# Kernel tuning notes

Hardware: AMD Instinct MI355X
Metric: run time of the kernel (lower is better)

The kernel has to match this reference:

```python
import jax, jax.numpy as jnp
import numpy as np

D = 512          # d_model
S = D // 2       # d_state
NL = 6           # num_layers
EVERY = 4        # attention_every
WIN = 256        # window_size
H = 8            # num_heads
DH = D // H      # head_dim
EPS = 1e-5


def layer_norm(x, gamma, beta):
    mu = jnp.mean(x, axis=-1, keepdims=True)
    var = jnp.mean((x - mu) ** 2, axis=-1, keepdims=True)
    return (x - mu) * jax.lax.rsqrt(var + EPS) * gamma + beta


def mamba_layer(seq, state, conv_w, Wx, Wh, Wout, A):
    """Lightweight Mamba-style update returning a (B, D) state summary.

    causal depthwise conv (k=3) -> SiLU -> project to d_state -> diagonal
    linear SSM scan (computed in closed form since the decay is constant)
    -> read out final state back to d_model.
    """
    B, L, _ = seq.shape
    xp = jnp.pad(seq, ((0, 0), (2, 0), (0, 0)))  # causal pad, kernel 3
    x = conv_w[0] * xp[:, :L] + conv_w[1] * xp[:, 1:L + 1] + conv_w[2] * xp[:, 2:L + 2]
    x = jax.nn.silu(x)
    u = jnp.einsum('bld,ds->bls', x, Wx)          # (B, L, S)
    a = jax.nn.sigmoid(A)                          # (S,) decay in (0,1)
    powers = (L - 1) - jnp.arange(L, dtype=jnp.float32)  # (L,)
    w = a[None, :] ** powers[:, None]              # (L, S)
    h0 = state @ Wh                                # (B, S)
    hT = (a ** L) * h0 + jnp.einsum('bls,ls->bs', u, w)
    return hT @ Wout                               # (B, D)


def local_attention(seq, Wqkv, bqkv, Wo, bo):
    B, L, _ = seq.shape
    qkv = seq @ Wqkv.T + bqkv                      # (B, L, 3D)
    q, k, v = jnp.split(qkv, 3, axis=-1)
    q = q.reshape(B, L, H, DH).transpose(0, 2, 1, 3)
    k = k.reshape(B, L, H, DH).transpose(0, 2, 1, 3)
    v = v.reshape(B, L, H, DH).transpose(0, 2, 1, 3)
    idx = jnp.arange(L)
    band = jnp.abs(idx[:, None] - idx[None, :]) <= WIN
    mask = jnp.where(band, 0.0, -jnp.inf).astype(seq.dtype)  # (L, L)
    scores = jnp.einsum('bhqd,bhkd->bhqk', q, k) / np.sqrt(DH) + mask
    attn = jax.nn.softmax(scores, axis=-1)
    out = jnp.einsum('bhqk,bhkd->bhqd', attn, v)
    out = out.transpose(0, 2, 1, 3).reshape(B, L, D)
    return out @ Wo.T + bo


def setup_inputs() -> dict:
    key = jax.random.key(0)
    ks = jax.random.split(key, 12)
    B, L = 4, 2048
    sc = 0.02
    return {
        'context': jax.random.normal(ks[0], (B, L, D), jnp.float32),
        'conv_w': jax.random.normal(ks[1], (NL, 3, D), jnp.float32) * sc,
        'Wx': jax.random.normal(ks[2], (NL, D, S), jnp.float32) * sc,
        'Wh': jax.random.normal(ks[3], (NL, D, S), jnp.float32) * sc,
        'Wout': jax.random.normal(ks[4], (NL, S, D), jnp.float32) * sc,
        'A': jax.random.normal(ks[5], (NL, S), jnp.float32),
        'gamma_m': jnp.ones((D,), jnp.float32),
        'beta_m': jnp.zeros((D,), jnp.float32),
        'gamma_a': jnp.ones((D,), jnp.float32),
        'beta_a': jnp.zeros((D,), jnp.float32),
        'Wqkv': jax.random.normal(ks[6], (3 * D, D), jnp.float32) * sc,
        'bqkv': jnp.zeros((3 * D,), jnp.float32),
        'Wo': jax.random.normal(ks[7], (D, D), jnp.float32) * sc,
        'bo': jnp.zeros((D,), jnp.float32),
    }


def reference(context, conv_w, Wx, Wh, Wout, A, gamma_m, beta_m, gamma_a, beta_a, Wqkv, bqkv, Wo, bo):
    B = context.shape[0]
    seq = context
    state = jnp.zeros((B, D), context.dtype)  # initial_state=None
    for i in range(NL):
        state = mamba_layer(seq, state, conv_w[i], Wx[i], Wh[i], Wout[i], A[i])
        seq = layer_norm(seq + state[:, None, :], gamma_m, beta_m)
        if (i + 1) % EVERY == 0:
            attn_out = local_attention(seq, Wqkv, bqkv, Wo, bo)
            seq = layer_norm(seq + attn_out, gamma_a, beta_a)
    return seq
```

## Files before the change

### kernel.cpp

```cpp
#include <hip/hip_runtime.h>

#define B_ 4
#define L_ 2048
#define D_ 512
#define S_ 256
#define H_ 8
#define DH_ 64
#define WIN_ 256
#define EPS_ 1e-5f
#define LOG2E_ 1.4426950408889634f
#define UWIN_ 768
#define UCHUNKS_ 6

using f32x4 = __attribute__((ext_vector_type(4))) float;
using s16x8 = __attribute__((ext_vector_type(8))) short;

__device__ __forceinline__ unsigned short f2b(float f) {
  unsigned int u = __builtin_bit_cast(unsigned int, f);
  u += 0x7FFFu + ((u >> 16) & 1u);
  return (unsigned short)(u >> 16);
}

__device__ __forceinline__ float silu(float y) { return y / (1.f + expf(-y)); }

__device__ __forceinline__ void gll16(const void* g, void* l) {
  __builtin_amdgcn_global_load_lds((const __attribute__((address_space(1))) void*)g,
                                   (__attribute__((address_space(3))) void*)l, 16, 0, 0);
}

__global__ __launch_bounds__(256) void k_f2b(const float* __restrict__ in,
                                             unsigned short* __restrict__ out, int n4) {
  int i = blockIdx.x * 256 + threadIdx.x;
  if (i >= n4) return;
  float4 v = reinterpret_cast<const float4*>(in)[i];
  ushort4 o;
  o.x = f2b(v.x); o.y = f2b(v.y); o.z = f2b(v.z); o.w = f2b(v.w);
  reinterpret_cast<ushort4*>(out)[i] = o;
}

__global__ void k_twx(const float* __restrict__ wx, unsigned short* __restrict__ wxt) {
  __shared__ float tile[32][33];
  int lyr = blockIdx.z;
  int d0 = blockIdx.x * 32, s0 = blockIdx.y * 32;
  const float* src = wx + (size_t)lyr * D_ * S_;
  unsigned short* dst = wxt + (size_t)lyr * S_ * D_;
  for (int r = threadIdx.y; r < 32; r += 8)
    tile[r][threadIdx.x] = src[(size_t)(d0 + r) * S_ + s0 + threadIdx.x];
  __syncthreads();
  for (int r = threadIdx.y; r < 32; r += 8)
    dst[(size_t)(s0 + r) * D_ + d0 + threadIdx.x] = f2b(tile[threadIdx.x][r]);
}

__global__ __launch_bounds__(128) void k_conv_silu(const float* __restrict__ seq,
                                                   const float* __restrict__ cw,
                                                   unsigned short* __restrict__ x) {
  int bl = blockIdx.x;
  int l = bl & (L_ - 1);
  int t = threadIdx.x;
  const float4* s4 = reinterpret_cast<const float4*>(seq);
  const float4* c4 = reinterpret_cast<const float4*>(cw);
  size_t row = (size_t)bl * 128;
  float4 c0 = c4[t], c1 = c4[128 + t], c2 = c4[256 + t];
  float4 z = make_float4(0.f, 0.f, 0.f, 0.f);
  float4 s0 = (l >= 2) ? s4[row - 256 + t] : z;
  float4 s1 = (l >= 1) ? s4[row - 128 + t] : z;
  float4 s2 = s4[row + t];
  float y0 = c0.x * s0.x + c1.x * s1.x + c2.x * s2.x;
  float y1 = c0.y * s0.y + c1.y * s1.y + c2.y * s2.y;
  float y2 = c0.z * s0.z + c1.z * s1.z + c2.z * s2.z;
  float y3 = c0.w * s0.w + c1.w * s1.w + c2.w * s2.w;
  ushort4 o;
  o.x = f2b(silu(y0)); o.y = f2b(silu(y1)); o.z = f2b(silu(y2)); o.w = f2b(silu(y3));
  reinterpret_cast<ushort4*>(x)[row + t] = o;
}

__global__ __launch_bounds__(64) void k_lnconv(const float* __restrict__ seqIn,
                                               const float* __restrict__ add, int addfull,
                                               const float* __restrict__ gamma,
                                               const float* __restrict__ beta,
                                               float* __restrict__ seqOut,
                                               unsigned short* __restrict__ xbf,
                                               const float* __restrict__ cw,
                                               unsigned short* __restrict__ sbf) {
  int t = threadIdx.x;
  int r0 = blockIdx.x * 8;
  int b = r0 >> 11, l0 = r0 & (L_ - 1);
  bool hasconv = (cw != nullptr);
  const float4* in4 = reinterpret_cast<const float4*>(seqIn);
  const float4* ad4 = reinterpret_cast<const float4*>(add);
  float4* out4 = reinterpret_cast<float4*>(seqOut);
  float4 g0 = reinterpret_cast<const float4*>(gamma)[2 * t];
  float4 g1 = reinterpret_cast<const float4*>(gamma)[2 * t + 1];
  float4 be0 = reinterpret_cast<const float4*>(beta)[2 * t];
  float4 be1 = reinterpret_cast<const float4*>(beta)[2 * t + 1];
  float4 av0, av1;
  if (!addfull) { av0 = ad4[b * 128 + 2 * t]; av1 = ad4[b * 128 + 2 * t + 1]; }
  float4 c0a, c0b, c1a, c1b, c2a, c2b;
  if (hasconv) {
    const float4* c4 = reinterpret_cast<const float4*>(cw);
    c0a = c4[2 * t]; c0b = c4[2 * t + 1];
    c1a = c4[128 + 2 * t]; c1b = c4[128 + 2 * t + 1];
    c2a = c4[256 + 2 * t]; c2b = c4[256 + 2 * t + 1];
  }
  float4 z = make_float4(0.f, 0.f, 0.f, 0.f);
  float4 m2a = z, m2b = z, m1a = z, m1b = z;
  int nrows = hasconv ? 10 : 8;
  int lstart = hasconv ? l0 - 2 : l0;
  for (int j = 0; j < nrows; ++j) {
    int l = lstart + j;
    float4 oa = z, ob = z;
    if (l >= 0) {
      size_t r4 = ((size_t)(b * L_ + l)) * 128;
      float4 v0 = in4[r4 + 2 * t], v1 = in4[r4 + 2 * t + 1];
      float4 a0, a1;
      if (addfull) { a0 = ad4[r4 + 2 * t]; a1 = ad4[r4 + 2 * t + 1]; }
      else { a0 = av0; a1 = av1; }
      v0.x += a0.x; v0.y += a0.y; v0.z += a0.z; v0.w += a0.w;
      v1.x += a1.x; v1.y += a1.y; v1.z += a1.z; v1.w += a1.w;
      float sx = v0.x + v0.y + v0.z + v0.w + v1.x + v1.y + v1.z + v1.w;
      float sq = v0.x * v0.x + v0.y * v0.y + v0.z * v0.z + v0.w * v0.w +
                 v1.x * v1.x + v1.y * v1.y + v1.z * v1.z + v1.w * v1.w;
#pragma unroll
      for (int off = 1; off < 64; off <<= 1) {
        sx += __shfl_xor(sx, off);
        sq += __shfl_xor(sq, off);
      }
      float mu = sx * (1.f / D_);
      float var = sq * (1.f / D_) - mu * mu;
      float rstd = rsqrtf(var + EPS_);
      oa.x = (v0.x - mu) * rstd * g0.x + be0.x;
      oa.y = (v0.y - mu) * rstd * g0.y + be0.y;
      oa.z = (v0.z - mu) * rstd * g0.z + be0.z;
      oa.w = (v0.w - mu) * rstd * g0.w + be0.w;
      ob.x = (v1.x - mu) * rstd * g1.x + be1.x;
      ob.y = (v1.y - mu) * rstd * g1.y + be1.y;
      ob.z = (v1.z - mu) * rstd * g1.z + be1.z;
      ob.w = (v1.w - mu) * rstd * g1.w + be1.w;
      if (l >= l0) {
        out4[r4 + 2 * t] = oa;
        out4[r4 + 2 * t + 1] = ob;
        if (sbf) {
          s16x8 sb;
          sb[0] = (short)f2b(oa.x); sb[1] = (short)f2b(oa.y);
          sb[2] = (short)f2b(oa.z); sb[3] = (short)f2b(oa.w);
          sb[4] = (short)f2b(ob.x); sb[5] = (short)f2b(ob.y);
          sb[6] = (short)f2b(ob.z); sb[7] = (short)f2b(ob.w);
          *reinterpret_cast<s16x8*>(sbf + ((size_t)(b * L_ + l)) * 512 + t * 8) = sb;
        }
      }
    }
    if (hasconv && j >= 2) {
      float y0 = c0a.x * m2a.x + c1a.x * m1a.x + c2a.x * oa.x;
      float y1 = c0a.y * m2a.y + c1a.y * m1a.y + c2a.y * oa.y;
      float y2 = c0a.z * m2a.z + c1a.z * m1a.z + c2a.z * oa.z;
      float y3 = c0a.w * m2a.w + c1a.w * m1a.w + c2a.w * oa.w;
      float y4 = c0b.x * m2b.x + c1b.x * m1b.x + c2b.x * ob.x;
      float y5 = c0b.y * m2b.y + c1b.y * m1b.y + c2b.y * ob.y;
      float y6 = c0b.z * m2b.z + c1b.z * m1b.z + c2b.z * ob.z;
      float y7 = c0b.w * m2b.w + c1b.w * m1b.w + c2b.w * ob.w;
      s16x8 xo;
      xo[0] = (short)f2b(silu(y0)); xo[1] = (short)f2b(silu(y1));
      xo[2] = (short)f2b(silu(y2)); xo[3] = (short)f2b(silu(y3));
      xo[4] = (short)f2b(silu(y4)); xo[5] = (short)f2b(silu(y5));
      xo[6] = (short)f2b(silu(y6)); xo[7] = (short)f2b(silu(y7));
      *reinterpret_cast<s16x8*>(xbf + ((size_t)(b * L_ + l)) * 512 + t * 8) = xo;
    }
    m2a = m1a; m2b = m1b; m1a = oa; m1b = ob;
  }
}

__device__ __forceinline__ void g128_core(const unsigned short* __restrict__ A,
                                          const unsigned short* __restrict__ Bt,
                                          int K, int m0, int n0, int k_lo, int k_hi,
                                          unsigned short* As, unsigned short* Bs,
                                          f32x4 (&acc)[4][4]) {
  int t = threadIdx.x;
  int lane = t & 63;
  int g = lane >> 4, mr = lane & 15;
  int wid = t >> 6, wr = wid >> 1, wc = wid & 1;
#pragma unroll
  for (int i = 0; i < 4; ++i)
#pragma unroll
    for (int j = 0; j < 4; ++j) { f32x4 z = {0.f, 0.f, 0.f, 0.f}; acc[i][j] = z; }
  int r0 = t >> 2, c4 = t & 3;
  int p = ((c4 ^ (r0 & 3)) << 3);
  const unsigned short* ag0 = A + (size_t)(m0 + r0) * K + p;
  const unsigned short* ag1 = ag0 + (size_t)64 * K;
  const unsigned short* bg0 = Bt + (size_t)(n0 + r0) * K + p;
  const unsigned short* bg1 = bg0 + (size_t)64 * K;
  int woff = wid * 512;
  int sa = ((g ^ (mr & 3)) << 3);
  gll16(ag0 + k_lo, As + woff);
  gll16(ag1 + k_lo, As + 2048 + woff);
  gll16(bg0 + k_lo, Bs + woff);
  gll16(bg1 + k_lo, Bs + 2048 + woff);
  int nsteps = (k_hi - k_lo) >> 5;
  int cur = 0;
  for (int s = 0; s < nsteps; ++s) {
    int k0 = k_lo + (s << 5);
    if (s + 1 < nsteps) {
      int nb = (cur ^ 1) * 4096;
      gll16(ag0 + k0 + 32, As + nb + woff);
      gll16(ag1 + k0 + 32, As + nb + 2048 + woff);
      gll16(bg0 + k0 + 32, Bs + nb + woff);
      gll16(bg1 + k0 + 32, Bs + nb + 2048 + woff);
      asm volatile("s_waitcnt vmcnt(4)" ::: "memory");
    } else {
      asm volatile("s_waitcnt vmcnt(0)" ::: "memory");
    }
    __builtin_amdgcn_sched_barrier(0);
    __builtin_amdgcn_s_barrier();
    __builtin_amdgcn_sched_barrier(0);
    const unsigned short* Ar = As + cur * 4096;
    const unsigned short* Br = Bs + cur * 4096;
    s16x8 af[4], bf[4];
#pragma unroll
    for (int fm = 0; fm < 4; ++fm)
      af[fm] = *reinterpret_cast<const s16x8*>(Ar + (size_t)(wr * 64 + fm * 16 + mr) * 32 + sa);
#pragma unroll
    for (int fn = 0; fn < 4; ++fn)
      bf[fn] = *reinterpret_cast<const s16x8*>(Br + (size_t)(wc * 64 + fn * 16 + mr) * 32 + sa);
#pragma unroll
    for (int fm = 0; fm < 4; ++fm)
#pragma unroll
      for (int fn = 0; fn < 4; ++fn)
        acc[fm][fn] = __builtin_amdgcn_mfma_f32_16x16x32_bf16(af[fm], bf[fn], acc[fm][fn], 0, 0, 0);
    __builtin_amdgcn_sched_barrier(0);
    __builtin_amdgcn_s_barrier();
    cur ^= 1;
  }
}

__global__ __launch_bounds__(256) void k_g128(const unsigned short* __restrict__ A,
                                              const unsigned short* __restrict__ Bt,
                                              float* __restrict__ C,
                                              const float* __restrict__ bias,
                                              int N, int K) {
  __shared__ __align__(16) unsigned short As[8192], Bs[8192];
  int m0 = blockIdx.x * 128, n0 = blockIdx.y * 128;
  f32x4 acc[4][4];
  g128_core(A, Bt, K, m0, n0, 0, K, As, Bs, acc);
  int t = threadIdx.x, lane = t & 63, g = lane >> 4, mr = lane & 15;
  int wid = t >> 6, wr = wid >> 1, wc = wid & 1;
#pragma unroll
  for (int fm = 0; fm < 4; ++fm)
#pragma unroll
    for (int fn = 0; fn < 4; ++fn) {
      int row = m0 + wr * 64 + fm * 16 + g * 4;
      int col = n0 + wc * 64 + fn * 16 + mr;
      float badd = bias ? bias[col] : 0.f;
#pragma unroll
      for (int q = 0; q < 4; ++q)
        C[(size_t)(row + q) * N + col] = acc[fm][fn][q] + badd;
    }
}

__global__ __launch_bounds__(256) void k_g128_qkv(const unsigned short* __restrict__ A,
                                                  const unsigned short* __restrict__ Bt,
                                                  const float* __restrict__ bias,
                                                  unsigned short* __restrict__ Qbf,
                                                  unsigned short* __restrict__ Kbf,
                                                  unsigned short* __restrict__ VbfT) {
  __shared__ __align__(16) unsigned short sm[16384];
  int m0 = blockIdx.x * 128, n0 = blockIdx.y * 128;
  f32x4 acc[4][4];
  g128_core(A, Bt, 512, m0, n0, 0, 512, sm, sm + 8192, acc);
  int t = threadIdx.x, lane = t & 63, g = lane >> 4, mr = lane & 15;
  int wid = t >> 6, wr = wid >> 1, wc = wid & 1;
  int b = m0 >> 11, l0 = m0 & (L_ - 1);
  if (n0 < 1024) {
#pragma unroll
    for (int fm = 0; fm < 4; ++fm)
#pragma unroll
      for (int fn = 0; fn < 4; ++fn) {
        int row0 = m0 + wr * 64 + fm * 16 + g * 4;
        int col = n0 + wc * 64 + fn * 16 + mr;
        int sec = col >> 9;
        int hh = (col >> 6) & 7;
        int dh = col & 63;
        float badd = bias[col];
        float scale = (sec == 0) ? 0.125f : 1.f;
        unsigned short* dstbase = (sec == 0) ? Qbf : Kbf;
#pragma unroll
        for (int q = 0; q < 4; ++q) {
          int row = row0 + q;
          int bb = row >> 11, l = row & (L_ - 1);
          dstbase[(((size_t)(bb * H_ + hh)) * L_ + l) * 64 + dh] =
              f2b((acc[fm][fn][q] + badd) * scale);
        }
      }
  } else {
#pragma unroll
    for (int chalf = 0; chalf < 2; ++chalf) {
      __syncthreads();
      if (wc == chalf) {
#pragma unroll
        for (int fm = 0; fm < 4; ++fm)
#pragma unroll
          for (int fn = 0; fn < 4; ++fn) {
            int col = n0 + wc * 64 + fn * 16 + mr;
            float badd = bias[col];
            int col_local = fn * 16 + mr;
            int row_local = wr * 64 + fm * 16 + g * 4;
            ushort4 pk;
            pk.x = f2b(acc[fm][fn][0] + badd);
            pk.y = f2b(acc[fm][fn][1] + badd);
            pk.z = f2b(acc[fm][fn][2] + badd);
            pk.w = f2b(acc[fm][fn][3] + badd);
            *reinterpret_cast<ushort4*>(&sm[col_local * 128 + row_local]) = pk;
          }
      }
      __syncthreads();
      int c = t >> 2, lp = (t & 3) * 32;
      int h = ((n0 - 1024) >> 6) + chalf;
      unsigned short* dst = VbfT + (((size_t)(b * H_ + h)) * 64 + c) * L_ + l0 + lp;
#pragma unroll
      for (int u = 0; u < 4; ++u)
        *reinterpret_cast<s16x8*>(dst + u * 8) =
            *reinterpret_cast<const s16x8*>(&sm[c * 128 + lp + u * 8]);
    }
  }
}

__global__ __launch_bounds__(256) void k_g128_u(const unsigned short* __restrict__ A,
                                                const unsigned short* __restrict__ Bt,
                                                const float* __restrict__ Ap,
                                                float* __restrict__ part3) {
  __shared__ __align__(16) unsigned short As[8192], Bs[8192];
  int mt = blockIdx.x;
  int b = mt / UCHUNKS_, cc = mt % UCHUNKS_;
  int m0 = b * L_ + (L_ - UWIN_) + cc * 128;
  int n0 = blockIdx.y * 128;
  int kz = blockIdx.z;
  f32x4 acc[4][4];
  g128_core(A, Bt, 512, m0, n0, kz * 128, kz * 128 + 128, As, Bs, acc);
  int t = threadIdx.x, lane = t & 63, g = lane >> 4, mr = lane & 15;
  int wid = t >> 6, wr = wid >> 1, wc = wid & 1;
  float wsum[4];
#pragma unroll
  for (int fn = 0; fn < 4; ++fn) {
    int col = n0 + wc * 64 + fn * 16 + mr;
    float a = 1.f / (1.f + expf(-Ap[col]));
    float la2 = log2f(a);
    float s = 0.f;
#pragma unroll
    for (int fm = 0; fm < 4; ++fm) {
      int rbase = (m0 + wr * 64 + fm * 16 + g * 4) & (L_ - 1);
#pragma unroll
      for (int q = 0; q < 4; ++q) {
        float e = (float)(2047 - (rbase + q));
        s += acc[fm][fn][q] * exp2f(e * la2);
      }
    }
    s += __shfl_xor(s, 16);
    s += __shfl_xor(s, 32);
    wsum[fn] = s;
  }
  float* red = (float*)As;
  __syncthreads();
  if (wr == 0 && g == 0) {
#pragma unroll
    for (int fn = 0; fn < 4; ++fn) red[(wc * 4 + fn) * 16 + mr] = wsum[fn];
  }
  __syncthreads();
  if (wr == 1 && g == 0) {
#pragma unroll
    for (int fn = 0; fn < 4; ++fn) {
      int col = n0 + wc * 64 + fn * 16 + mr;
      part3[(((size_t)(b * UCHUNKS_ + cc)) * 4 + kz) * 256 + col] =
          wsum[fn] + red[(wc * 4 + fn) * 16 + mr];
    }
  }
}

__global__ __launch_bounds__(256) void k_tail(const float* __restrict__ part3,
                                              const float* __restrict__ Wout,
                                              float* __restrict__ state) {
  int bz = blockIdx.x;
  int b = bz >> 4, dl = (bz & 15) * 32;
  int t = threadIdx.x;
  __shared__ float hTs[256];
  __shared__ float red[8][33];
  float acc = 0.f;
#pragma unroll
  for (int c = 0; c < UCHUNKS_ * 4; ++c)
    acc += part3[((size_t)b * UCHUNKS_ * 4 + c) * 256 + t];
  hTs[t] = acc;
  __syncthreads();
  int dx = t & 31, sy = t >> 5;
  float p = 0.f;
  for (int j = 0; j < 32; ++j) {
    int s = sy * 32 + j;
    p += hTs[s] * Wout[(size_t)s * 512 + dl + dx];
  }
  red[sy][dx] = p;
  __syncthreads();
  if (t < 32) {
    float a = 0.f;
#pragma unroll
    for (int k = 0; k < 8; ++k) a += red[k][t];
    state[b * 512 + dl + t] = a;
  }
}

__global__ __launch_bounds__(256) void k_fattn(const unsigned short* __restrict__ Qbf,
                                               const unsigned short* __restrict__ Kbf,
                                               const unsigned short* __restrict__ VbfT,
                                               unsigned short* __restrict__ attnbf) {
  __shared__ __align__(16) unsigned short Ks[64][72];
  __shared__ __align__(16) unsigned short Vt[64][72];
  __shared__ __align__(16) unsigned short Ps[4][16][72];
  int b = blockIdx.z, h = blockIdx.y, q0 = blockIdx.x * 64;
  int t = threadIdx.x;
  int lane = t & 63, wid = t >> 6;
  int g = lane >> 4, mr = lane & 15;
  const unsigned short* Qp = Qbf + ((size_t)(b * H_ + h)) * L_ * 64;
  const unsigned short* Kp = Kbf + ((size_t)(b * H_ + h)) * L_ * 64;
  const unsigned short* VpT = VbfT + ((size_t)(b * H_ + h)) * 64 * L_;
  int qbase = q0 + wid * 16;
  s16x8 qf0 = *reinterpret_cast<const s16x8*>(Qp + (size_t)(qbase + mr) * 64 + g * 8);
  s16x8 qf1 = *reinterpret_cast<const s16x8*>(Qp + (size_t)(qbase + mr) * 64 + 32 + g * 8);
  f32x4 oacc[4];
#pragma unroll
  for (int fn = 0; fn < 4; ++fn) { f32x4 zz = {0.f, 0.f, 0.f, 0.f}; oacc[fn] = zz; }
  float lsum[4] = {0.f, 0.f, 0.f, 0.f};
  int kstart = q0 - WIN_; if (kstart < 0) kstart = 0;
  int kend = q0 + 64 + WIN_; if (kend > L_) kend = L_;

  for (int kt = kstart; kt < kend; kt += 64) {
    __syncthreads();
#pragma unroll
    for (int it = 0; it < 2; ++it) {
      int chunk = t + it * 256;
      int row = chunk >> 3, c8 = (chunk & 7) * 8;
      *reinterpret_cast<s16x8*>(&Ks[row][c8]) =
          *reinterpret_cast<const s16x8*>(Kp + (size_t)(kt + row) * 64 + c8);
      *reinterpret_cast<s16x8*>(&Vt[row][c8]) =
          *reinterpret_cast<const s16x8*>(VpT + (size_t)row * L_ + kt + c8);
    }
    __syncthreads();
    f32x4 sacc[4];
#pragma unroll
    for (int n = 0; n < 4; ++n) {
      f32x4 zz = {0.f, 0.f, 0.f, 0.f};
      sacc[n] = zz;
      s16x8 kf0 = *reinterpret_cast<const s16x8*>(&Ks[n * 16 + mr][g * 8]);
      s16x8 kf1 = *reinterpret_cast<const s16x8*>(&Ks[n * 16 + mr][32 + g * 8]);
      sacc[n] = __builtin_amdgcn_mfma_f32_16x16x32_bf16(qf0, kf0, sacc[n], 0, 0, 0);
      sacc[n] = __builtin_amdgcn_mfma_f32_16x16x32_bf16(qf1, kf1, sacc[n], 0, 0, 0);
    }
    bool needmask = (kt - q0 > 192) || (q0 - kt > 192);
#pragma unroll
    for (int reg = 0; reg < 4; ++reg) {
      int q_abs = qbase + g * 4 + reg;
#pragma unroll
      for (int n = 0; n < 4; ++n) {
        float pv = exp2f(sacc[n][reg] * LOG2E_);
        if (needmask) {
          int key = kt + n * 16 + mr;
          int dd = key - q_abs; dd = dd < 0 ? -dd : dd;
          if (dd > WIN_) pv = 0.f;
        }
        lsum[reg] += pv;
        Ps[wid][g * 4 + reg][n * 16 + mr] = f2b(pv);
      }
    }
    s16x8 pa0 = *reinterpret_cast<const s16x8*>(&Ps[wid][mr][g * 8]);
    s16x8 pa1 = *reinterpret_cast<const s16x8*>(&Ps[wid][mr][32 + g * 8]);
#pragma unroll
    for (int fn = 0; fn < 4; ++fn) {
      s16x8 vf0 = *reinterpret_cast<const s16x8*>(&Vt[fn * 16 + mr][g * 8]);
      s16x8 vf1 = *reinterpret_cast<const s16x8*>(&Vt[fn * 16 + mr][32 + g * 8]);
      oacc[fn] = __builtin_amdgcn_mfma_f32_16x16x32_bf16(pa0, vf0, oacc[fn], 0, 0, 0);
      oacc[fn] = __builtin_amdgcn_mfma_f32_16x16x32_bf16(pa1, vf1, oacc[fn], 0, 0, 0);
    }
  }
#pragma unroll
  for (int reg = 0; reg < 4; ++reg) {
    float ls = lsum[reg];
#pragma unroll
    for (int off = 1; off < 16; off <<= 1) ls += __shfl_xor(ls, off);
    float inv = 1.f / ls;
    int q_abs = qbase + g * 4 + reg;
    unsigned short* dst = attnbf + ((size_t)(b * L_ + q_abs)) * 512 + h * 64;
#pragma unroll
    for (int fn = 0; fn < 4; ++fn)
      dst[fn * 16 + mr] = f2b(oacc[fn][reg] * inv);
  }
}

extern "C" void kernel_launch(void* const* d_in, const int* in_sizes, int n_in,
                              void* d_out, int out_size, void* d_ws, size_t ws_size,
                              hipStream_t stream) {
  const float* context = (const float*)d_in[0];
  const float* conv_w  = (const float*)d_in[1];
  const float* Wx      = (const float*)d_in[2];
  const float* Wout    = (const float*)d_in[4];
  const float* Aparm   = (const float*)d_in[5];
  const float* gamma_m = (const float*)d_in[6];
  const float* beta_m  = (const float*)d_in[7];
  const float* gamma_a = (const float*)d_in[8];
  const float* beta_a  = (const float*)d_in[9];
  const float* Wqkv    = (const float*)d_in[10];
  const float* bqkv    = (const float*)d_in[11];
  const float* Wo      = (const float*)d_in[12];
  const float* bo      = (const float*)d_in[13];
  float* seqA = (float*)d_out;
  float* ws = (float*)d_ws;

  float* proj = ws;
  float* seqB = ws + 4194304;
  unsigned short* Qbf    = (unsigned short*)(ws + 4194304);
  unsigned short* Kbf    = (unsigned short*)(ws + 6291456);
  unsigned short* VbfT   = (unsigned short*)(ws + 8388608);
  unsigned short* xbf    = (unsigned short*)(ws + 10485760);
  unsigned short* sbf    = (unsigned short*)(ws + 12582912);
  unsigned short* wqkvbf = (unsigned short*)(ws + 14680064);
  unsigned short* wobf   = (unsigned short*)(ws + 15073280);
  unsigned short* wxtbf  = (unsigned short*)(ws + 15204352);
  float* state = ws + 15597568;
  float* part3 = state + 2048;

  k_f2b<<<768, 256, 0, stream>>>(Wqkv, wqkvbf, 196608);
  k_f2b<<<256, 256, 0, stream>>>(Wo, wobf, 65536);
  k_twx<<<dim3(16, 8, 6), dim3(32, 8), 0, stream>>>(Wx, wxtbf);

  k_conv_silu<<<B_ * L_, 128, 0, stream>>>(context, conv_w, xbf);

  for (int i = 0; i < 6; ++i) {
    k_g128_u<<<dim3(B_ * UCHUNKS_, 2, 4), 256, 0, stream>>>(
        xbf, wxtbf + (size_t)i * S_ * D_, Aparm + (size_t)i * S_, part3);
    k_tail<<<64, 256, 0, stream>>>(part3, Wout + (size_t)i * S_ * D_, state);
    const float* cwn = conv_w + (size_t)(i + 1) * 3 * D_;
    switch (i) {
      case 0:
        k_lnconv<<<1024, 64, 0, stream>>>(context, state, 0, gamma_m, beta_m,
                                          seqA, xbf, cwn, nullptr);
        break;
      case 1:
        k_lnconv<<<1024, 64, 0, stream>>>(seqA, state, 0, gamma_m, beta_m,
                                          seqB, xbf, cwn, nullptr);
        break;
      case 2:
        k_lnconv<<<1024, 64, 0, stream>>>(seqB, state, 0, gamma_m, beta_m,
                                          seqA, xbf, cwn, nullptr);
        break;
      case 3:
        k_lnconv<<<1024, 64, 0, stream>>>(seqA, state, 0, gamma_m, beta_m,
                                          seqA, nullptr, nullptr, sbf);
        k_g128_qkv<<<dim3(64, 12), 256, 0, stream>>>(sbf, wqkvbf, bqkv, Qbf, Kbf, VbfT);
        k_fattn<<<dim3(32, 8, 4), 256, 0, stream>>>(Qbf, Kbf, VbfT, sbf);
        k_g128<<<dim3(64, 4), 256, 0, stream>>>(sbf, wobf, proj, bo, 512, 512);
        k_lnconv<<<1024, 64, 0, stream>>>(seqA, proj, 1, gamma_a, beta_a,
                                          seqB, xbf, cwn, nullptr);
        break;
      case 4:
        k_lnconv<<<1024, 64, 0, stream>>>(seqB, state, 0, gamma_m, beta_m,
                                          seqA, xbf, cwn, nullptr);
        break;
      case 5:
        k_lnconv<<<1024, 64, 0, stream>>>(seqA, state, 0, gamma_m, beta_m,
                                          seqA, nullptr, nullptr, nullptr);
        break;
    }
  }
}
```

Measured before the change: 258.9 us.

## Store intermediate sequence in bf16, add XCD block remap, drop LDS swizzle

The residual sequence between layers is now stored as bf16 rather than fp32. The final layer writes fp32 to the output. This halves the traffic of the layernorm/conv kernels, but the residual stream accumulates bf16 rounding across layers. The GEMM kernels also get a 1D grid with XCD-aware block remapping, lose the XOR LDS swizzle (which may bring back bank conflicts), and pad the QKV transpose staging to a stride of 136.

```diff
diff --git a/kernel.cpp b/kernel.cpp
--- a/kernel.cpp
+++ b/kernel.cpp
@@ -19,6 +19,9 @@
   unsigned int u = __builtin_bit_cast(unsigned int, f);
   u += 0x7FFFu + ((u >> 16) & 1u);
   return (unsigned short)(u >> 16);
+}
+__device__ __forceinline__ float b2f(unsigned short u) {
+  return __builtin_bit_cast(float, (unsigned int)u << 16);
 }
 
 __device__ __forceinline__ float silu(float y) { return y / (1.f + expf(-y)); }
@@ -74,21 +77,21 @@
   reinterpret_cast<ushort4*>(x)[row + t] = o;
 }
 
-__global__ __launch_bounds__(64) void k_lnconv(const float* __restrict__ seqIn,
+__global__ __launch_bounds__(64) void k_lnconv(const void* __restrict__ seqIn, int in_bf16,
                                                const float* __restrict__ add, int addfull,
                                                const float* __restrict__ gamma,
                                                const float* __restrict__ beta,
-                                               float* __restrict__ seqOut,
+                                               unsigned short* __restrict__ outBf,
+                                               float* __restrict__ outF32,
                                                unsigned short* __restrict__ xbf,
-                                               const float* __restrict__ cw,
-                                               unsigned short* __restrict__ sbf) {
+                                               const float* __restrict__ cw) {
   int t = threadIdx.x;
   int r0 = blockIdx.x * 8;
   int b = r0 >> 11, l0 = r0 & (L_ - 1);
   bool hasconv = (cw != nullptr);
   const float4* in4 = reinterpret_cast<const float4*>(seqIn);
+  const s16x8* inb = reinterpret_cast<const s16x8*>(seqIn);
   const float4* ad4 = reinterpret_cast<const float4*>(add);
-  float4* out4 = reinterpret_cast<float4*>(seqOut);
   float4 g0 = reinterpret_cast<const float4*>(gamma)[2 * t];
   float4 g1 = reinterpret_cast<const float4*>(gamma)[2 * t + 1];
   float4 be0 = reinterpret_cast<const float4*>(beta)[2 * t];
@@ -111,7 +114,16 @@
     float4 oa = z, ob = z;
     if (l >= 0) {
       size_t r4 = ((size_t)(b * L_ + l)) * 128;
-      float4 v0 = in4[r4 + 2 * t], v1 = in4[r4 + 2 * t + 1];
+      float4 v0, v1;
+      if (in_bf16) {
+        s16x8 v8 = inb[((size_t)(b * L_ + l)) * 64 + t];
+        v0.x = b2f((unsigned short)v8[0]); v0.y = b2f((unsigned short)v8[1]);
+        v0.z = b2f((unsigned short)v8[2]); v0.w = b2f((unsigned short)v8[3]);
+        v1.x = b2f((unsigned short)v8[4]); v1.y = b2f((unsigned short)v8[5]);
+        v1.z = b2f((unsigned short)v8[6]); v1.w = b2f((unsigned short)v8[7]);
+      } else {
+        v0 = in4[r4 + 2 * t]; v1 = in4[r4 + 2 * t + 1];
+      }
       float4 a0, a1;
       if (addfull) { a0 = ad4[r4 + 2 * t]; a1 = ad4[r4 + 2 * t + 1]; }
       else { a0 = av0; a1 = av1; }
@@ -137,15 +149,18 @@
       ob.z = (v1.z - mu) * rstd * g1.z + be1.z;
       ob.w = (v1.w - mu) * rstd * g1.w + be1.w;
       if (l >= l0) {
-        out4[r4 + 2 * t] = oa;
-        out4[r4 + 2 * t + 1] = ob;
-        if (sbf) {
+        if (outBf) {
           s16x8 sb;
           sb[0] = (short)f2b(oa.x); sb[1] = (short)f2b(oa.y);
           sb[2] = (short)f2b(oa.z); sb[3] = (short)f2b(oa.w);
           sb[4] = (short)f2b(ob.x); sb[5] = (short)f2b(ob.y);
           sb[6] = (short)f2b(ob.z); sb[7] = (short)f2b(ob.w);
-          *reinterpret_cast<s16x8*>(sbf + ((size_t)(b * L_ + l)) * 512 + t * 8) = sb;
+          *reinterpret_cast<s16x8*>(outBf + ((size_t)(b * L_ + l)) * 512 + t * 8) = sb;
+        }
+        if (outF32) {
+          float4* o4 = reinterpret_cast<float4*>(outF32);
+          o4[r4 + 2 * t] = oa;
+          o4[r4 + 2 * t + 1] = ob;
         }
       }
     }
@@ -182,14 +197,12 @@
   for (int i = 0; i < 4; ++i)
 #pragma unroll
     for (int j = 0; j < 4; ++j) { f32x4 z = {0.f, 0.f, 0.f, 0.f}; acc[i][j] = z; }
-  int r0 = t >> 2, c4 = t & 3;
-  int p = ((c4 ^ (r0 & 3)) << 3);
+  int r0 = t >> 2, p = (t & 3) * 8;
   const unsigned short* ag0 = A + (size_t)(m0 + r0) * K + p;
   const unsigned short* ag1 = ag0 + (size_t)64 * K;
   const unsigned short* bg0 = Bt + (size_t)(n0 + r0) * K + p;
   const unsigned short* bg1 = bg0 + (size_t)64 * K;
   int woff = wid * 512;
-  int sa = ((g ^ (mr & 3)) << 3);
   gll16(ag0 + k_lo, As + woff);
   gll16(ag1 + k_lo, As + 2048 + woff);
   gll16(bg0 + k_lo, Bs + woff);
@@ -216,10 +229,10 @@
     s16x8 af[4], bf[4];
 #pragma unroll
     for (int fm = 0; fm < 4; ++fm)
-      af[fm] = *reinterpret_cast<const s16x8*>(Ar + (size_t)(wr * 64 + fm * 16 + mr) * 32 + sa);
+      af[fm] = *reinterpret_cast<const s16x8*>(Ar + (size_t)(wr * 64 + fm * 16 + mr) * 32 + g * 8);
 #pragma unroll
     for (int fn = 0; fn < 4; ++fn)
-      bf[fn] = *reinterpret_cast<const s16x8*>(Br + (size_t)(wc * 64 + fn * 16 + mr) * 32 + sa);
+      bf[fn] = *reinterpret_cast<const s16x8*>(Br + (size_t)(wc * 64 + fn * 16 + mr) * 32 + g * 8);
 #pragma unroll
     for (int fm = 0; fm < 4; ++fm)
 #pragma unroll
@@ -231,13 +244,18 @@
   }
 }
 
+__device__ __forceinline__ int xcd_lb(int bid, int nwg) {
+  return (bid & 7) * (nwg >> 3) + (bid >> 3);
+}
+
 __global__ __launch_bounds__(256) void k_g128(const unsigned short* __restrict__ A,
                                               const unsigned short* __restrict__ Bt,
                                               float* __restrict__ C,
                                               const float* __restrict__ bias,
-                                              int N, int K) {
+                                              int N, int K, int ntn) {
   __shared__ __align__(16) unsigned short As[8192], Bs[8192];
-  int m0 = blockIdx.x * 128, n0 = blockIdx.y * 128;
+  int lb = xcd_lb(blockIdx.x, gridDim.x);
+  int m0 = (lb / ntn) * 128, n0 = (lb % ntn) * 128;
   f32x4 acc[4][4];
   g128_core(A, Bt, K, m0, n0, 0, K, As, Bs, acc);
   int t = threadIdx.x, lane = t & 63, g = lane >> 4, mr = lane & 15;
@@ -262,7 +280,8 @@
                                                   unsigned short* __restrict__ Kbf,
                                                   unsigned short* __restrict__ VbfT) {
   __shared__ __align__(16) unsigned short sm[16384];
-  int m0 = blockIdx.x * 128, n0 = blockIdx.y * 128;
+  int lb = xcd_lb(blockIdx.x, gridDim.x);
+  int m0 = (lb / 12) * 128, n0 = (lb % 12) * 128;
   f32x4 acc[4][4];
   g128_core(A, Bt, 512, m0, n0, 0, 512, sm, sm + 8192, acc);
   int t = threadIdx.x, lane = t & 63, g = lane >> 4, mr = lane & 15;
@@ -307,7 +326,7 @@
             pk.y = f2b(acc[fm][fn][1] + badd);
             pk.z = f2b(acc[fm][fn][2] + badd);
             pk.w = f2b(acc[fm][fn][3] + badd);
-            *reinterpret_cast<ushort4*>(&sm[col_local * 128 + row_local]) = pk;
+            *reinterpret_cast<ushort4*>(&sm[col_local * 136 + row_local]) = pk;
           }
       }
       __syncthreads();
@@ -317,7 +336,7 @@
 #pragma unroll
       for (int u = 0; u < 4; ++u)
         *reinterpret_cast<s16x8*>(dst + u * 8) =
-            *reinterpret_cast<const s16x8*>(&sm[c * 128 + lp + u * 8]);
+            *reinterpret_cast<const s16x8*>(&sm[c * 136 + lp + u * 8]);
     }
   }
 }
@@ -327,11 +346,13 @@
                                                 const float* __restrict__ Ap,
                                                 float* __restrict__ part3) {
   __shared__ __align__(16) unsigned short As[8192], Bs[8192];
-  int mt = blockIdx.x;
+  int lb = xcd_lb(blockIdx.x, gridDim.x);
+  int mt = lb >> 3;
+  int rr = lb & 7;
+  int nt = rr >> 2, kz = rr & 3;
   int b = mt / UCHUNKS_, cc = mt % UCHUNKS_;
   int m0 = b * L_ + (L_ - UWIN_) + cc * 128;
-  int n0 = blockIdx.y * 128;
-  int kz = blockIdx.z;
+  int n0 = nt * 128;
   f32x4 acc[4][4];
   g128_core(A, Bt, 512, m0, n0, kz * 128, kz * 128 + 128, As, Bs, acc);
   int t = threadIdx.x, lane = t & 63, g = lane >> 4, mr = lane & 15;
@@ -505,16 +526,17 @@
   const float* bqkv    = (const float*)d_in[11];
   const float* Wo      = (const float*)d_in[12];
   const float* bo      = (const float*)d_in[13];
-  float* seqA = (float*)d_out;
+  float* outF = (float*)d_out;
   float* ws = (float*)d_ws;
 
   float* proj = ws;
-  float* seqB = ws + 4194304;
-  unsigned short* Qbf    = (unsigned short*)(ws + 4194304);
-  unsigned short* Kbf    = (unsigned short*)(ws + 6291456);
+  unsigned short* Qbf    = (unsigned short*)(ws);
+  unsigned short* Kbf    = (unsigned short*)(ws + 2097152);
+  unsigned short* seqAb  = (unsigned short*)(ws + 4194304);
+  unsigned short* seqBb  = (unsigned short*)(ws + 6291456);
   unsigned short* VbfT   = (unsigned short*)(ws + 8388608);
   unsigned short* xbf    = (unsigned short*)(ws + 10485760);
-  unsigned short* sbf    = (unsigned short*)(ws + 12582912);
+  unsigned short* attnbf = (unsigned short*)(ws + 12582912);
   unsigned short* wqkvbf = (unsigned short*)(ws + 14680064);
   unsigned short* wobf   = (unsigned short*)(ws + 15073280);
   unsigned short* wxtbf  = (unsigned short*)(ws + 15204352);
@@ -528,39 +550,39 @@
   k_conv_silu<<<B_ * L_, 128, 0, stream>>>(context, conv_w, xbf);
 
   for (int i = 0; i < 6; ++i) {
-    k_g128_u<<<dim3(B_ * UCHUNKS_, 2, 4), 256, 0, stream>>>(
+    k_g128_u<<<B_ * UCHUNKS_ * 8, 256, 0, stream>>>(
         xbf, wxtbf + (size_t)i * S_ * D_, Aparm + (size_t)i * S_, part3);
     k_tail<<<64, 256, 0, stream>>>(part3, Wout + (size_t)i * S_ * D_, state);
     const float* cwn = conv_w + (size_t)(i + 1) * 3 * D_;
     switch (i) {
       case 0:
-        k_lnconv<<<1024, 64, 0, stream>>>(context, state, 0, gamma_m, beta_m,
-                                          seqA, xbf, cwn, nullptr);
+        k_lnconv<<<1024, 64, 0, stream>>>(context, 0, state, 0, gamma_m, beta_m,
+                                          seqAb, nullptr, xbf, cwn);
         break;
       case 1:
-        k_lnconv<<<1024, 64, 0, stream>>>(seqA, state, 0, gamma_m, beta_m,
-                                          seqB, xbf, cwn, nullptr);
+        k_lnconv<<<1024, 64, 0, stream>>>(seqAb, 1, state, 0, gamma_m, beta_m,
+                                          seqBb, nullptr, xbf, cwn);
         break;
       case 2:
-        k_lnconv<<<1024, 64, 0, stream>>>(seqB, state, 0, gamma_m, beta_m,
-                                          seqA, xbf, cwn, nullptr);
+        k_lnconv<<<1024, 64, 0, stream>>>(seqBb, 1, state, 0, gamma_m, beta_m,
+                                          seqAb, nullptr, xbf, cwn);
         break;
       case 3:
-        k_lnconv<<<1024, 64, 0, stream>>>(seqA, state, 0, gamma_m, beta_m,
-                                          seqA, nullptr, nullptr, sbf);
-        k_g128_qkv<<<dim3(64, 12), 256, 0, stream>>>(sbf, wqkvbf, bqkv, Qbf, Kbf, VbfT);
-        k_fattn<<<dim3(32, 8, 4), 256, 0, stream>>>(Qbf, Kbf, VbfT, sbf);
-        k_g128<<<dim3(64, 4), 256, 0, stream>>>(sbf, wobf, proj, bo, 512, 512);
-        k_lnconv<<<1024, 64, 0, stream>>>(seqA, proj, 1, gamma_a, beta_a,
-                                          seqB, xbf, cwn, nullptr);
+        k_lnconv<<<1024, 64, 0, stream>>>(seqAb, 1, state, 0, gamma_m, beta_m,
+                                          seqAb, nullptr, nullptr, nullptr);
+        k_g128_qkv<<<768, 256, 0, stream>>>(seqAb, wqkvbf, bqkv, Qbf, Kbf, VbfT);
+        k_fattn<<<dim3(32, 8, 4), 256, 0, stream>>>(Qbf, Kbf, VbfT, attnbf);
+        k_g128<<<256, 256, 0, stream>>>(attnbf, wobf, proj, bo, 512, 512, 4);
+        k_lnconv<<<1024, 64, 0, stream>>>(seqAb, 1, proj, 1, gamma_a, beta_a,
+                                          seqBb, nullptr, xbf, cwn);
         break;
       case 4:
-        k_lnconv<<<1024, 64, 0, stream>>>(seqB, state, 0, gamma_m, beta_m,
-                                          seqA, xbf, cwn, nullptr);
+        k_lnconv<<<1024, 64, 0, stream>>>(seqBb, 1, state, 0, gamma_m, beta_m,
+                                          seqAb, nullptr, xbf, cwn);
         break;
       case 5:
-        k_lnconv<<<1024, 64, 0, stream>>>(seqA, state, 0, gamma_m, beta_m,
-                                          seqA, nullptr, nullptr, nullptr);
+        k_lnconv<<<1024, 64, 0, stream>>>(seqAb, 1, state, 0, gamma_m, beta_m,
+                                          nullptr, outF, nullptr, nullptr);
         break;
     }
   }
```

After: 257.8 us. About the same (-0.4%).
